# Performance work log

Measured on AMD Instinct MI355X. Metric: run time of the kernel, lower is better.

Reference implementation:

```python
import jax, jax.numpy as jnp
import numpy as np

D_MODEL = 1024
EXPANSION = 4
NUM_TILES = 4
D_FF = D_MODEL * EXPANSION


def setup_inputs() -> dict:
    key = jax.random.key(0)
    k1, k2, k3, k4, k5 = jax.random.split(key, 5)
    x = jax.random.normal(k1, (8, 2048, D_MODEL), dtype=jnp.float32)
    w_up = jax.random.normal(k2, (D_FF, D_MODEL), dtype=jnp.float32) * 0.02
    b_up = jax.random.normal(k3, (D_FF,), dtype=jnp.float32) * 0.02
    w_down = jax.random.normal(k4, (D_MODEL, D_FF), dtype=jnp.float32) * 0.02
    b_down = jax.random.normal(k5, (D_MODEL,), dtype=jnp.float32) * 0.02
    return {"x": x, "w_up": w_up, "b_up": b_up, "w_down": w_down, "b_down": b_down}


def reference(x, w_up, b_up, w_down, b_down):
    B, T, C = x.shape
    xf = x.reshape(B * T, C)  # [N, d_model]
    N = B * T

    # Emergent tile signatures: sign of per-tile row sums of up_proj weight.
    tile_up = D_FF // NUM_TILES
    signatures = jnp.sign(w_up.reshape(NUM_TILES, tile_up, C).sum(axis=1))  # [num_tiles, d_model]

    # Routing: argmax over input-signature alignment -> one-hot gate.
    scores = xf @ signatures.T                      # [N, num_tiles]
    winner = jnp.argmax(scores, axis=-1)            # [N]
    gate = jax.nn.one_hot(winner, NUM_TILES, dtype=xf.dtype)  # [N, num_tiles]

    # Tile-gated up projection (gate scales output tile blocks), then ReLU.
    hidden = xf @ w_up.T + b_up                     # [N, d_ff]
    hidden = (hidden.reshape(N, NUM_TILES, tile_up) * gate[:, :, None]).reshape(N, D_FF)
    hidden = jax.nn.relu(hidden)

    # Tile-gated down projection.
    tile_down = D_MODEL // NUM_TILES
    out = hidden @ w_down.T + b_down                # [N, d_model]
    out = (out.reshape(N, NUM_TILES, tile_down) * gate[:, :, None]).reshape(N, D_MODEL)

    return out.reshape(B, T, D_MODEL), gate.reshape(B, T, NUM_TILES)
```

## Files before the change

### kernel.cpp

```cpp
#include <hip/hip_runtime.h>
#include <stdint.h>
#include <stddef.h>

#define N_TOK 16384
#define DM    1024
#define DFF   4096
#define NT    4
#define TU    1024
#define TD    256

typedef __attribute__((ext_vector_type(8))) short  short8;
typedef __attribute__((ext_vector_type(4))) short  short4v;
typedef __attribute__((ext_vector_type(4))) float  floatx4;

__device__ inline unsigned short f2bf(float f){
  union { float f; uint32_t u; } v; v.f = f;
  uint32_t u = v.u + 0x7FFFu + ((v.u >> 16) & 1u);
  return (unsigned short)(u >> 16);
}

__device__ __forceinline__ void gll16(const void* g, void* l){
  __builtin_amdgcn_global_load_lds(
      (const __attribute__((address_space(1))) unsigned int*)g,
      (__attribute__((address_space(3))) unsigned int*)l,
      16, 0, 0);
}

__global__ void k_sig_partial(const float* __restrict__ w_up,
                              float* __restrict__ partial,
                              unsigned short* __restrict__ wupb){
  const int b = blockIdx.x, tid = threadIdx.x;
  const int tile = b >> 6, chunk = b & 63;
  const int c0 = tid * 4;
  const int row0 = tile*TU + chunk*16;
  float s0=0.f, s1=0.f, s2=0.f, s3=0.f;
  const float* base = w_up + (size_t)row0 * DM + c0;
  #pragma unroll
  for (int r = 0; r < 16; ++r){
    floatx4 v = *(const floatx4*)(base + (size_t)r * DM);
    s0 += v[0]; s1 += v[1]; s2 += v[2]; s3 += v[3];
    short4v p;
    p[0]=(short)f2bf(v[0]); p[1]=(short)f2bf(v[1]);
    p[2]=(short)f2bf(v[2]); p[3]=(short)f2bf(v[3]);
    *(short4v*)(wupb + (size_t)(row0 + r) * DM + c0) = p;
  }
  float* p = partial + ((size_t)tile*DM + c0) * 64 + chunk;
  p[0] = s0; p[64] = s1; p[128] = s2; p[192] = s3;
}

__global__ void k_sig_final(const float* __restrict__ partial,
                            float* __restrict__ sig){
  const int g = blockIdx.x * 256 + threadIdx.x;
  const float* p = partial + (size_t)g * 64;
  float s = 0.f;
  #pragma unroll
  for (int i = 0; i < 64; ++i) s += p[i];
  sig[g] = (s > 0.f) ? 1.f : ((s < 0.f) ? -1.f : 0.f);
}

__global__ void k_wdown_conv(const float* __restrict__ w,
                             unsigned short* __restrict__ wb){
  const size_t i = ((size_t)blockIdx.x * 256 + threadIdx.x) * 8;
  floatx4 v0 = *(const floatx4*)(w + i);
  floatx4 v1 = *(const floatx4*)(w + i + 4);
  short8 p;
  p[0]=(short)f2bf(v0[0]); p[1]=(short)f2bf(v0[1]); p[2]=(short)f2bf(v0[2]); p[3]=(short)f2bf(v0[3]);
  p[4]=(short)f2bf(v1[0]); p[5]=(short)f2bf(v1[1]); p[6]=(short)f2bf(v1[2]); p[7]=(short)f2bf(v1[3]);
  *(short8*)(wb + i) = p;
}

__global__ __launch_bounds__(256) void k_route(
    const float* __restrict__ x, const float* __restrict__ sig,
    float* __restrict__ gate_out, int* __restrict__ winner,
    unsigned short* __restrict__ xbf){
  __shared__ float ssig[NT * DM];
  const int tid = threadIdx.x;
  for (int i = tid; i < NT*DM; i += 256) ssig[i] = sig[i];
  __syncthreads();
  const int wv = tid >> 6, lane = tid & 63;
  const int n = blockIdx.x * 4 + wv;
  const float* xr = x + (size_t)n * DM;
  unsigned short* xb = xbf + (size_t)n * 2048 + 1024;
  double a0=0.0, a1=0.0, a2=0.0, a3=0.0;
  #pragma unroll
  for (int j = 0; j < 4; ++j){
    const int c = j*256 + lane*4;
    floatx4 v = *(const floatx4*)(xr + c);
    short4v p;
    p[0]=(short)f2bf(v[0]); p[1]=(short)f2bf(v[1]);
    p[2]=(short)f2bf(v[2]); p[3]=(short)f2bf(v[3]);
    *(short4v*)(xb + c) = p;
    #pragma unroll
    for (int u = 0; u < 4; ++u){
      double xv = (double)v[u];
      a0 += xv * (double)ssig[c+u];
      a1 += xv * (double)ssig[DM   + c+u];
      a2 += xv * (double)ssig[2*DM + c+u];
      a3 += xv * (double)ssig[3*DM + c+u];
    }
  }
  #pragma unroll
  for (int off = 32; off > 0; off >>= 1){
    a0 += __shfl_down(a0, off, 64);
    a1 += __shfl_down(a1, off, 64);
    a2 += __shfl_down(a2, off, 64);
    a3 += __shfl_down(a3, off, 64);
  }
  if (lane == 0){
    double s[4] = {a0, a1, a2, a3};
    int w = 0;
    #pragma unroll
    for (int t = 1; t < 4; ++t) if (s[t] > s[w]) w = t;
    floatx4 g = { w==0 ? 1.f:0.f, w==1 ? 1.f:0.f, w==2 ? 1.f:0.f, w==3 ? 1.f:0.f };
    *(floatx4*)(gate_out + (size_t)n * 4) = g;
    winner[n] = w;
  }
}

__global__ void k_hist(const int* __restrict__ winner,
                       int* __restrict__ blk_cnt){
  __shared__ int wcnt[4][NT];
  const int tid = threadIdx.x, wv = tid >> 6, lane = tid & 63;
  const int w = winner[blockIdx.x * 256 + tid];
  #pragma unroll
  for (int t = 0; t < NT; ++t){
    unsigned long long m = __ballot(w == t);
    if (lane == 0) wcnt[wv][t] = __popcll(m);
  }
  __syncthreads();
  if (tid < NT){
    int s = wcnt[0][tid] + wcnt[1][tid] + wcnt[2][tid] + wcnt[3][tid];
    blk_cnt[blockIdx.x * NT + tid] = s;
  }
}

__global__ void k_scan(const int* __restrict__ blk_cnt,
                       int* __restrict__ meta, int* __restrict__ blk_base){
  if (threadIdx.x == 0){
    int tot[NT] = {0,0,0,0};
    for (int b = 0; b < 64; ++b)
      for (int t = 0; t < NT; ++t) tot[t] += blk_cnt[b*NT + t];
    int off = 0;
    for (int t = 0; t < NT; ++t){ meta[t] = tot[t]; meta[4+t] = off; off += tot[t]; }
    int run[NT];
    for (int t = 0; t < NT; ++t) run[t] = meta[4+t];
    for (int b = 0; b < 64; ++b)
      for (int t = 0; t < NT; ++t){ blk_base[b*NT + t] = run[t]; run[t] += blk_cnt[b*NT + t]; }
  }
}

__global__ void k_scatter(const int* __restrict__ winner,
                          const int* __restrict__ blk_base,
                          int* __restrict__ idx){
  __shared__ int wcnt[4][NT];
  const int tid = threadIdx.x, wv = tid >> 6, lane = tid & 63;
  const int n = blockIdx.x * 256 + tid;
  const int w = winner[n];
  unsigned long long mymask = 0;
  #pragma unroll
  for (int t = 0; t < NT; ++t){
    unsigned long long m = __ballot(w == t);
    if (lane == 0) wcnt[wv][t] = __popcll(m);
    if (t == w) mymask = m;
  }
  __syncthreads();
  const unsigned long long below = (lane == 0) ? 0ull : (~0ull >> (64 - lane));
  int pos = blk_base[blockIdx.x * NT + w] + __popcll(mymask & below);
  for (int v = 0; v < wv; ++v) pos += wcnt[v][w];
  idx[pos] = n;
}

__global__ __launch_bounds__(256, 2) void k_gemm1(
    const unsigned short* __restrict__ xbf,
    const unsigned short* __restrict__ wupb,
    const float* __restrict__ b_up, const int* __restrict__ meta,
    const int* __restrict__ idx, unsigned short* __restrict__ hid){
  const int tile = blockIdx.z;
  const int cnt  = meta[tile];
  const int p0   = blockIdx.x * 128;
  if (p0 >= cnt) return;
  const int off  = meta[4 + tile];
  const int nb   = blockIdx.y;

  __shared__ unsigned short smem[8704];
  unsigned short* As = smem;
  unsigned short* Bs = smem + 4096;
  __shared__ int nrow[128];

  const int tid = threadIdx.x;
  if (tid < 128){
    int p = p0 + tid;
    nrow[tid] = idx[off + (p < cnt ? p : cnt - 1)];
  }
  __syncthreads();

  const int wv = tid >> 6, lane = tid & 63;
  const int wm = (wv >> 1) * 64, wn = (wv & 1) * 64;
  const int l16 = lane & 15, quad = lane >> 4;

  const int rsub = lane >> 2;
  const int kus  = (lane & 3) * 8;

  const int ra = wv*32 + rsub;
  const unsigned short* aptr0 = xbf + (size_t)nrow[ra]      * 2048 + 1024 + kus;
  const unsigned short* aptr1 = xbf + (size_t)nrow[ra + 16] * 2048 + 1024 + kus;
  const unsigned short* bptr0 = wupb + (size_t)(tile*TU + nb*128 + wv*32 + rsub) * DM + kus;
  const unsigned short* bptr1 = bptr0 + 16 * DM;

  unsigned short* asd0 = As + (wv*32) * 32;
  unsigned short* asd1 = asd0 + 16 * 32;
  unsigned short* bsd0 = Bs + (wv*32) * 32;
  unsigned short* bsd1 = bsd0 + 16 * 32;

  floatx4 acc[4][4];
  #pragma unroll
  for (int i = 0; i < 4; ++i)
    #pragma unroll
    for (int j = 0; j < 4; ++j) acc[i][j] = (floatx4){0.f,0.f,0.f,0.f};

  for (int k0 = 0; k0 < DM; k0 += 32){
    gll16(aptr0, asd0);
    gll16(aptr1, asd1);
    gll16(bptr0, bsd0);
    gll16(bptr1, bsd1);
    aptr0 += 32; aptr1 += 32; bptr0 += 32; bptr1 += 32;
    __syncthreads();
    short8 af[4], bfr[4];
    #pragma unroll
    for (int i = 0; i < 4; ++i) af[i]  = *(const short8*)(As + (wm + i*16 + l16)*32 + quad*8);
    #pragma unroll
    for (int j = 0; j < 4; ++j) bfr[j] = *(const short8*)(Bs + (wn + j*16 + l16)*32 + quad*8);
    #pragma unroll
    for (int i = 0; i < 4; ++i)
      #pragma unroll
      for (int j = 0; j < 4; ++j)
        acc[i][j] = __builtin_amdgcn_mfma_f32_16x16x32_bf16(af[i], bfr[j], acc[i][j], 0, 0, 0);
    __syncthreads();
  }

  const int gcol0 = nb*128;
  #pragma unroll
  for (int half = 0; half < 2; ++half){
    if ((wv >> 1) == half){
      #pragma unroll
      for (int i = 0; i < 4; ++i){
        #pragma unroll
        for (int j = 0; j < 4; ++j){
          const int col = wn + j*16 + l16;
          const float bias = b_up[tile*TU + gcol0 + col];
          #pragma unroll
          for (int r = 0; r < 4; ++r){
            const int lrow = i*16 + quad*4 + r;
            float v = acc[i][j][r] + bias;
            smem[lrow*136 + col] = f2bf(v > 0.f ? v : 0.f);
          }
        }
      }
    }
    __syncthreads();
    #pragma unroll
    for (int c = tid; c < 1024; c += 256){
      const int lrow = c >> 4, k8 = (c & 15) * 8;
      const int m = half*64 + lrow;
      if (p0 + m < cnt){
        short8 vv = *(const short8*)(smem + lrow*136 + k8);
        *(short8*)(hid + (size_t)nrow[m]*2048 + gcol0 + k8) = vv;
      }
    }
    __syncthreads();
  }
}

__global__ __launch_bounds__(256, 2) void k_gemm2(
    const unsigned short* __restrict__ hid,
    const unsigned short* __restrict__ wdownb,
    const float* __restrict__ b_down, const int* __restrict__ meta,
    const int* __restrict__ idx, float* __restrict__ out){
  const int tile = blockIdx.z;
  const int cnt  = meta[tile];
  const int p0   = blockIdx.x * 32;
  if (p0 >= cnt) return;
  const int off  = meta[4 + tile];

  __shared__ unsigned short smem[9216];
  unsigned short* As = smem;
  unsigned short* Bs = smem + 1024;
  float* epi = (float*)smem;
  __shared__ int nrow[32];

  const int tid = threadIdx.x;
  if (tid < 32){
    int p = p0 + tid;
    nrow[tid] = idx[off + (p < cnt ? p : cnt - 1)];
  }
  __syncthreads();

  const int wv = tid >> 6, lane = tid & 63;
  const int wn = wv * 64;
  const int l16 = lane & 15, quad = lane >> 4;

  const int rsub = lane >> 2;
  const int kus  = (lane & 3) * 8;

  const unsigned short* aptr = hid + (size_t)nrow[(wv & 1)*16 + rsub] * 2048 + kus;
  unsigned short* asd = As + ((wv & 1)*16) * 32;
  const unsigned short* bptr = wdownb + (size_t)(tile*TD + wv*64 + rsub) * DFF + tile*TU + kus;
  unsigned short* bsd = Bs + (wv*64) * 32;

  floatx4 acc[2][4];
  #pragma unroll
  for (int i = 0; i < 2; ++i)
    #pragma unroll
    for (int j = 0; j < 4; ++j) acc[i][j] = (floatx4){0.f,0.f,0.f,0.f};

  for (int k0 = 0; k0 < TU; k0 += 32){
    if (wv < 2) gll16(aptr, asd);
    gll16(bptr,          bsd);
    gll16(bptr + 16*DFF, bsd + 16*32);
    gll16(bptr + 32*DFF, bsd + 32*32);
    gll16(bptr + 48*DFF, bsd + 48*32);
    aptr += 32; bptr += 32;
    __syncthreads();
    short8 af[2], bfr[4];
    #pragma unroll
    for (int i = 0; i < 2; ++i) af[i]  = *(const short8*)(As + (i*16 + l16)*32 + quad*8);
    #pragma unroll
    for (int j = 0; j < 4; ++j) bfr[j] = *(const short8*)(Bs + (wn + j*16 + l16)*32 + quad*8);
    #pragma unroll
    for (int i = 0; i < 2; ++i)
      #pragma unroll
      for (int j = 0; j < 4; ++j)
        acc[i][j] = __builtin_amdgcn_mfma_f32_16x16x32_bf16(af[i], bfr[j], acc[i][j], 0, 0, 0);
    __syncthreads();
  }

  #pragma unroll
  for (int half = 0; half < 2; ++half){
    #pragma unroll
    for (int j = 0; j < 4; ++j){
      const int col = wn + j*16 + l16;
      const float bias = b_down[tile*TD + col];
      #pragma unroll
      for (int r = 0; r < 4; ++r){
        const int lrow = quad*4 + r;
        epi[lrow*260 + col] = acc[half][j][r] + bias;
      }
    }
    __syncthreads();
    #pragma unroll
    for (int c = tid; c < 1024; c += 256){
      const int lrow = c >> 6, c4 = (c & 63) * 4;
      const int m = half*16 + lrow;
      if (p0 + m < cnt){
        floatx4 v = *(const floatx4*)(epi + lrow*260 + c4);
        *(floatx4*)(out + (size_t)nrow[m]*DM + tile*TD + c4) = v;
      }
    }
    __syncthreads();
  }
}

__global__ void k_zero(const int* __restrict__ winner, float* __restrict__ out){
  const int tid = threadIdx.x;
  const int tok = blockIdx.x * 16 + (tid >> 4);
  const int sub = tid & 15;
  const int w = winner[tok];
  float* row = out + (size_t)tok * DM;
  const floatx4 z = {0.f, 0.f, 0.f, 0.f};
  #pragma unroll
  for (int cb = 0; cb < 4; ++cb){
    if (cb == w) continue;
    float* p = row + cb*256 + sub*16;
    *(floatx4*)(p)      = z;
    *(floatx4*)(p + 4)  = z;
    *(floatx4*)(p + 8)  = z;
    *(floatx4*)(p + 12) = z;
  }
}

extern "C" void kernel_launch(void* const* d_in, const int* in_sizes, int n_in,
                              void* d_out, int out_size, void* d_ws, size_t ws_size,
                              hipStream_t stream){
  const float* x      = (const float*)d_in[0];
  const float* w_up   = (const float*)d_in[1];
  const float* b_up   = (const float*)d_in[2];
  const float* w_down = (const float*)d_in[3];
  const float* b_down = (const float*)d_in[4];

  unsigned short* wupb   = (unsigned short*)d_ws;
  unsigned short* wdownb = wupb + (size_t)DFF * DM;
  float* partial = (float*)(wdownb + (size_t)DM * DFF);
  float* sig     = partial + 262144;
  int*   ints    = (int*)(sig + 4096);
  int*   winner   = ints;
  int*   idx      = ints + 16384;
  int*   meta     = ints + 32768;
  int*   blk_cnt  = ints + 32776;
  int*   blk_base = ints + 33032;

  float*          out  = (float*)d_out;
  float*          gate = out + (size_t)N_TOK * DM;
  unsigned short* ob16 = (unsigned short*)d_out;

  k_sig_partial<<<dim3(NT*64), 256, 0, stream>>>(w_up, partial, wupb);
  k_sig_final  <<<dim3(16),    256, 0, stream>>>(partial, sig);
  k_wdown_conv <<<dim3(2048),  256, 0, stream>>>(w_down, wdownb);
  k_route      <<<dim3(N_TOK/4), 256, 0, stream>>>(x, sig, gate, winner, ob16);
  k_hist       <<<dim3(64),    256, 0, stream>>>(winner, blk_cnt);
  k_scan       <<<dim3(1),      64, 0, stream>>>(blk_cnt, meta, blk_base);
  k_scatter    <<<dim3(64),    256, 0, stream>>>(winner, blk_base, idx);
  k_gemm1      <<<dim3(128, 8, NT), 256, 0, stream>>>(ob16, wupb, b_up, meta, idx, ob16);
  k_gemm2      <<<dim3(512, 1, NT), 256, 0, stream>>>(ob16, wdownb, b_down, meta, idx, out);
  k_zero       <<<dim3(N_TOK/16), 256, 0, stream>>>(winner, out);
}
```

Baseline: 299.5 us.

## Load MFMA fragments directly from global memory, fuse zero-fill into gemm2

Both GEMM kernels drop the LDS staging through global_load_lds and instead have each wave load its MFMA A/B fragments straight from global memory with per-row pointers, removing the per-iteration barriers. The k_zero kernel is folded into gemm2, which now zeroes the non-winning column blocks of each routed row, saving one launch and a separate pass over the output. gemm1's grid is transposed so blocks sharing a token tile are adjacent, which should improve L2 reuse of gathered activations. The cost is that operand reuse across waves now depends on cache instead of shared memory, which risks more global traffic.

Result: slower. 442.5 us (+47.7%).

```diff
diff --git a/kernel.cpp b/kernel.cpp
--- a/kernel.cpp
+++ b/kernel.cpp
@@ -17,13 +17,6 @@
   union { float f; uint32_t u; } v; v.f = f;
   uint32_t u = v.u + 0x7FFFu + ((v.u >> 16) & 1u);
   return (unsigned short)(u >> 16);
-}
-
-__device__ __forceinline__ void gll16(const void* g, void* l){
-  __builtin_amdgcn_global_load_lds(
-      (const __attribute__((address_space(1))) unsigned int*)g,
-      (__attribute__((address_space(3))) unsigned int*)l,
-      16, 0, 0);
 }
 
 __global__ void k_sig_partial(const float* __restrict__ w_up,
@@ -177,14 +170,12 @@
     const int* __restrict__ idx, unsigned short* __restrict__ hid){
   const int tile = blockIdx.z;
   const int cnt  = meta[tile];
-  const int p0   = blockIdx.x * 128;
+  const int p0   = blockIdx.y * 128;
   if (p0 >= cnt) return;
   const int off  = meta[4 + tile];
-  const int nb   = blockIdx.y;
-
-  __shared__ unsigned short smem[8704];
-  unsigned short* As = smem;
-  unsigned short* Bs = smem + 4096;
+  const int nb   = blockIdx.x;
+
+  __shared__ unsigned short epi[64 * 136];
   __shared__ int nrow[128];
 
   const int tid = threadIdx.x;
@@ -198,19 +189,14 @@
   const int wm = (wv >> 1) * 64, wn = (wv & 1) * 64;
   const int l16 = lane & 15, quad = lane >> 4;
 
-  const int rsub = lane >> 2;
-  const int kus  = (lane & 3) * 8;
-
-  const int ra = wv*32 + rsub;
-  const unsigned short* aptr0 = xbf + (size_t)nrow[ra]      * 2048 + 1024 + kus;
-  const unsigned short* aptr1 = xbf + (size_t)nrow[ra + 16] * 2048 + 1024 + kus;
-  const unsigned short* bptr0 = wupb + (size_t)(tile*TU + nb*128 + wv*32 + rsub) * DM + kus;
-  const unsigned short* bptr1 = bptr0 + 16 * DM;
-
-  unsigned short* asd0 = As + (wv*32) * 32;
-  unsigned short* asd1 = asd0 + 16 * 32;
-  unsigned short* bsd0 = Bs + (wv*32) * 32;
-  unsigned short* bsd1 = bsd0 + 16 * 32;
+  const unsigned short* aP[4];
+  #pragma unroll
+  for (int i = 0; i < 4; ++i)
+    aP[i] = xbf + (size_t)nrow[wm + i*16 + l16] * 2048 + 1024 + quad*8;
+  const unsigned short* bP[4];
+  #pragma unroll
+  for (int j = 0; j < 4; ++j)
+    bP[j] = wupb + (size_t)(tile*TU + nb*128 + wn + j*16 + l16) * DM + quad*8;
 
   floatx4 acc[4][4];
   #pragma unroll
@@ -218,24 +204,18 @@
     #pragma unroll
     for (int j = 0; j < 4; ++j) acc[i][j] = (floatx4){0.f,0.f,0.f,0.f};
 
+  #pragma unroll 2
   for (int k0 = 0; k0 < DM; k0 += 32){
-    gll16(aptr0, asd0);
-    gll16(aptr1, asd1);
-    gll16(bptr0, bsd0);
-    gll16(bptr1, bsd1);
-    aptr0 += 32; aptr1 += 32; bptr0 += 32; bptr1 += 32;
-    __syncthreads();
     short8 af[4], bfr[4];
     #pragma unroll
-    for (int i = 0; i < 4; ++i) af[i]  = *(const short8*)(As + (wm + i*16 + l16)*32 + quad*8);
-    #pragma unroll
-    for (int j = 0; j < 4; ++j) bfr[j] = *(const short8*)(Bs + (wn + j*16 + l16)*32 + quad*8);
+    for (int i = 0; i < 4; ++i) af[i]  = *(const short8*)(aP[i] + k0);
+    #pragma unroll
+    for (int j = 0; j < 4; ++j) bfr[j] = *(const short8*)(bP[j] + k0);
     #pragma unroll
     for (int i = 0; i < 4; ++i)
       #pragma unroll
       for (int j = 0; j < 4; ++j)
         acc[i][j] = __builtin_amdgcn_mfma_f32_16x16x32_bf16(af[i], bfr[j], acc[i][j], 0, 0, 0);
-    __syncthreads();
   }
 
   const int gcol0 = nb*128;
@@ -252,7 +232,7 @@
           for (int r = 0; r < 4; ++r){
             const int lrow = i*16 + quad*4 + r;
             float v = acc[i][j][r] + bias;
-            smem[lrow*136 + col] = f2bf(v > 0.f ? v : 0.f);
+            epi[lrow*136 + col] = f2bf(v > 0.f ? v : 0.f);
           }
         }
       }
@@ -263,7 +243,7 @@
       const int lrow = c >> 4, k8 = (c & 15) * 8;
       const int m = half*64 + lrow;
       if (p0 + m < cnt){
-        short8 vv = *(const short8*)(smem + lrow*136 + k8);
+        short8 vv = *(const short8*)(epi + lrow*136 + k8);
         *(short8*)(hid + (size_t)nrow[m]*2048 + gcol0 + k8) = vv;
       }
     }
@@ -282,10 +262,7 @@
   if (p0 >= cnt) return;
   const int off  = meta[4 + tile];
 
-  __shared__ unsigned short smem[9216];
-  unsigned short* As = smem;
-  unsigned short* Bs = smem + 1024;
-  float* epi = (float*)smem;
+  __shared__ float epi[16 * 260];
   __shared__ int nrow[32];
 
   const int tid = threadIdx.x;
@@ -299,13 +276,14 @@
   const int wn = wv * 64;
   const int l16 = lane & 15, quad = lane >> 4;
 
-  const int rsub = lane >> 2;
-  const int kus  = (lane & 3) * 8;
-
-  const unsigned short* aptr = hid + (size_t)nrow[(wv & 1)*16 + rsub] * 2048 + kus;
-  unsigned short* asd = As + ((wv & 1)*16) * 32;
-  const unsigned short* bptr = wdownb + (size_t)(tile*TD + wv*64 + rsub) * DFF + tile*TU + kus;
-  unsigned short* bsd = Bs + (wv*64) * 32;
+  const unsigned short* aP[2];
+  #pragma unroll
+  for (int i = 0; i < 2; ++i)
+    aP[i] = hid + (size_t)nrow[i*16 + l16] * 2048 + quad*8;
+  const unsigned short* bP[4];
+  #pragma unroll
+  for (int j = 0; j < 4; ++j)
+    bP[j] = wdownb + (size_t)(tile*TD + wn + j*16 + l16) * DFF + tile*TU + quad*8;
 
   floatx4 acc[2][4];
   #pragma unroll
@@ -313,25 +291,31 @@
     #pragma unroll
     for (int j = 0; j < 4; ++j) acc[i][j] = (floatx4){0.f,0.f,0.f,0.f};
 
+  #pragma unroll 2
   for (int k0 = 0; k0 < TU; k0 += 32){
-    if (wv < 2) gll16(aptr, asd);
-    gll16(bptr,          bsd);
-    gll16(bptr + 16*DFF, bsd + 16*32);
-    gll16(bptr + 32*DFF, bsd + 32*32);
-    gll16(bptr + 48*DFF, bsd + 48*32);
-    aptr += 32; bptr += 32;
-    __syncthreads();
     short8 af[2], bfr[4];
     #pragma unroll
-    for (int i = 0; i < 2; ++i) af[i]  = *(const short8*)(As + (i*16 + l16)*32 + quad*8);
-    #pragma unroll
-    for (int j = 0; j < 4; ++j) bfr[j] = *(const short8*)(Bs + (wn + j*16 + l16)*32 + quad*8);
+    for (int i = 0; i < 2; ++i) af[i]  = *(const short8*)(aP[i] + k0);
+    #pragma unroll
+    for (int j = 0; j < 4; ++j) bfr[j] = *(const short8*)(bP[j] + k0);
     #pragma unroll
     for (int i = 0; i < 2; ++i)
       #pragma unroll
       for (int j = 0; j < 4; ++j)
         acc[i][j] = __builtin_amdgcn_mfma_f32_16x16x32_bf16(af[i], bfr[j], acc[i][j], 0, 0, 0);
-    __syncthreads();
+  }
+
+  __syncthreads();
+
+  const floatx4 z4 = {0.f, 0.f, 0.f, 0.f};
+  #pragma unroll
+  for (int cb = 0; cb < 4; ++cb){
+    if (cb == tile) continue;
+    for (int c = tid; c < 32*64; c += 256){
+      const int rowl = c >> 6, c4 = (c & 63) * 4;
+      if (p0 + rowl < cnt)
+        *(floatx4*)(out + (size_t)nrow[rowl]*DM + cb*256 + c4) = z4;
+    }
   }
 
   #pragma unroll
@@ -357,24 +341,6 @@
       }
     }
     __syncthreads();
-  }
-}
-
-__global__ void k_zero(const int* __restrict__ winner, float* __restrict__ out){
-  const int tid = threadIdx.x;
-  const int tok = blockIdx.x * 16 + (tid >> 4);
-  const int sub = tid & 15;
-  const int w = winner[tok];
-  float* row = out + (size_t)tok * DM;
-  const floatx4 z = {0.f, 0.f, 0.f, 0.f};
-  #pragma unroll
-  for (int cb = 0; cb < 4; ++cb){
-    if (cb == w) continue;
-    float* p = row + cb*256 + sub*16;
-    *(floatx4*)(p)      = z;
-    *(floatx4*)(p + 4)  = z;
-    *(floatx4*)(p + 8)  = z;
-    *(floatx4*)(p + 12) = z;
   }
 }
 
@@ -409,7 +375,6 @@
   k_hist       <<<dim3(64),    256, 0, stream>>>(winner, blk_cnt);
   k_scan       <<<dim3(1),      64, 0, stream>>>(blk_cnt, meta, blk_base);
   k_scatter    <<<dim3(64),    256, 0, stream>>>(winner, blk_base, idx);
-  k_gemm1      <<<dim3(128, 8, NT), 256, 0, stream>>>(ob16, wupb, b_up, meta, idx, ob16);
+  k_gemm1      <<<dim3(8, 128, NT), 256, 0, stream>>>(ob16, wupb, b_up, meta, idx, ob16);
   k_gemm2      <<<dim3(512, 1, NT), 256, 0, stream>>>(ob16, wdownb, b_down, meta, idx, out);
-  k_zero       <<<dim3(N_TOK/16), 256, 0, stream>>>(winner, out);
-}
+}
```

## Double the gemm1 K step per barrier and fold output zeroing into gemm2

Applied to the files above, without the earlier changes.

The first grouped GEMM now loads two 32-wide K slices into separate LDS buffers per iteration, which halves the number of barrier pairs per K loop at the cost of doubled shared memory (32 KB). The separate zeroing kernel is removed. Each gemm2 block now writes zeros to the three non-winning output column tiles of its own rows, which saves one launch and the winner re-read. The larger LDS footprint may reduce occupancy under the two-block launch bound.

Measured after the change: 283.1 us. -5.5%, faster.

```diff
diff --git a/kernel.cpp b/kernel.cpp
--- a/kernel.cpp
+++ b/kernel.cpp
@@ -182,9 +182,11 @@
   const int off  = meta[4 + tile];
   const int nb   = blockIdx.y;
 
-  __shared__ unsigned short smem[8704];
-  unsigned short* As = smem;
-  unsigned short* Bs = smem + 4096;
+  __shared__ unsigned short smem[16384];
+  unsigned short* As0 = smem;
+  unsigned short* As1 = smem + 4096;
+  unsigned short* Bs0 = smem + 8192;
+  unsigned short* Bs1 = smem + 12288;
   __shared__ int nrow[128];
 
   const int tid = threadIdx.x;
@@ -207,10 +209,10 @@
   const unsigned short* bptr0 = wupb + (size_t)(tile*TU + nb*128 + wv*32 + rsub) * DM + kus;
   const unsigned short* bptr1 = bptr0 + 16 * DM;
 
-  unsigned short* asd0 = As + (wv*32) * 32;
-  unsigned short* asd1 = asd0 + 16 * 32;
-  unsigned short* bsd0 = Bs + (wv*32) * 32;
-  unsigned short* bsd1 = bsd0 + 16 * 32;
+  unsigned short* a0d0 = As0 + (wv*32) * 32;  unsigned short* a0d1 = a0d0 + 16*32;
+  unsigned short* a1d0 = As1 + (wv*32) * 32;  unsigned short* a1d1 = a1d0 + 16*32;
+  unsigned short* b0d0 = Bs0 + (wv*32) * 32;  unsigned short* b0d1 = b0d0 + 16*32;
+  unsigned short* b1d0 = Bs1 + (wv*32) * 32;  unsigned short* b1d1 = b1d0 + 16*32;
 
   floatx4 acc[4][4];
   #pragma unroll
@@ -218,23 +220,40 @@
     #pragma unroll
     for (int j = 0; j < 4; ++j) acc[i][j] = (floatx4){0.f,0.f,0.f,0.f};
 
-  for (int k0 = 0; k0 < DM; k0 += 32){
-    gll16(aptr0, asd0);
-    gll16(aptr1, asd1);
-    gll16(bptr0, bsd0);
-    gll16(bptr1, bsd1);
-    aptr0 += 32; aptr1 += 32; bptr0 += 32; bptr1 += 32;
-    __syncthreads();
-    short8 af[4], bfr[4];
-    #pragma unroll
-    for (int i = 0; i < 4; ++i) af[i]  = *(const short8*)(As + (wm + i*16 + l16)*32 + quad*8);
-    #pragma unroll
-    for (int j = 0; j < 4; ++j) bfr[j] = *(const short8*)(Bs + (wn + j*16 + l16)*32 + quad*8);
-    #pragma unroll
-    for (int i = 0; i < 4; ++i)
-      #pragma unroll
-      for (int j = 0; j < 4; ++j)
-        acc[i][j] = __builtin_amdgcn_mfma_f32_16x16x32_bf16(af[i], bfr[j], acc[i][j], 0, 0, 0);
+  for (int k0 = 0; k0 < DM; k0 += 64){
+    gll16(aptr0 + k0,      a0d0);
+    gll16(aptr1 + k0,      a0d1);
+    gll16(aptr0 + k0 + 32, a1d0);
+    gll16(aptr1 + k0 + 32, a1d1);
+    gll16(bptr0 + k0,      b0d0);
+    gll16(bptr1 + k0,      b0d1);
+    gll16(bptr0 + k0 + 32, b1d0);
+    gll16(bptr1 + k0 + 32, b1d1);
+    __syncthreads();
+    {
+      short8 af[4], bfr[4];
+      #pragma unroll
+      for (int i = 0; i < 4; ++i) af[i]  = *(const short8*)(As0 + (wm + i*16 + l16)*32 + quad*8);
+      #pragma unroll
+      for (int j = 0; j < 4; ++j) bfr[j] = *(const short8*)(Bs0 + (wn + j*16 + l16)*32 + quad*8);
+      #pragma unroll
+      for (int i = 0; i < 4; ++i)
+        #pragma unroll
+        for (int j = 0; j < 4; ++j)
+          acc[i][j] = __builtin_amdgcn_mfma_f32_16x16x32_bf16(af[i], bfr[j], acc[i][j], 0, 0, 0);
+    }
+    {
+      short8 af[4], bfr[4];
+      #pragma unroll
+      for (int i = 0; i < 4; ++i) af[i]  = *(const short8*)(As1 + (wm + i*16 + l16)*32 + quad*8);
+      #pragma unroll
+      for (int j = 0; j < 4; ++j) bfr[j] = *(const short8*)(Bs1 + (wn + j*16 + l16)*32 + quad*8);
+      #pragma unroll
+      for (int i = 0; i < 4; ++i)
+        #pragma unroll
+        for (int j = 0; j < 4; ++j)
+          acc[i][j] = __builtin_amdgcn_mfma_f32_16x16x32_bf16(af[i], bfr[j], acc[i][j], 0, 0, 0);
+    }
     __syncthreads();
   }
 
@@ -334,6 +353,17 @@
     __syncthreads();
   }
 
+  const floatx4 z4 = {0.f, 0.f, 0.f, 0.f};
+  #pragma unroll
+  for (int cb = 0; cb < 4; ++cb){
+    if (cb == tile) continue;
+    for (int c = tid; c < 32*64; c += 256){
+      const int rowl = c >> 6, c4 = (c & 63) * 4;
+      if (p0 + rowl < cnt)
+        *(floatx4*)(out + (size_t)nrow[rowl]*DM + cb*256 + c4) = z4;
+    }
+  }
+
   #pragma unroll
   for (int half = 0; half < 2; ++half){
     #pragma unroll
@@ -357,24 +387,6 @@
       }
     }
     __syncthreads();
-  }
-}
-
-__global__ void k_zero(const int* __restrict__ winner, float* __restrict__ out){
-  const int tid = threadIdx.x;
-  const int tok = blockIdx.x * 16 + (tid >> 4);
-  const int sub = tid & 15;
-  const int w = winner[tok];
-  float* row = out + (size_t)tok * DM;
-  const floatx4 z = {0.f, 0.f, 0.f, 0.f};
-  #pragma unroll
-  for (int cb = 0; cb < 4; ++cb){
-    if (cb == w) continue;
-    float* p = row + cb*256 + sub*16;
-    *(floatx4*)(p)      = z;
-    *(floatx4*)(p + 4)  = z;
-    *(floatx4*)(p + 8)  = z;
-    *(floatx4*)(p + 12) = z;
   }
 }
 
@@ -411,5 +423,4 @@
   k_scatter    <<<dim3(64),    256, 0, stream>>>(winner, blk_base, idx);
   k_gemm1      <<<dim3(128, 8, NT), 256, 0, stream>>>(ob16, wupb, b_up, meta, idx, ob16);
   k_gemm2      <<<dim3(512, 1, NT), 256, 0, stream>>>(ob16, wdownb, b_down, meta, idx, out);
-  k_zero       <<<dim3(N_TOK/16), 256, 0, stream>>>(winner, out);
-}
+}
```
